# Optimization experiments

Measured on AMD Instinct MI355X. Metric: run time of the kernel, lower is better.

## Reference

```python
import jax, jax.numpy as jnp
import numpy as np

OUT, IN, BLK = 4096, 4096, 32
N_BLOCKS = OUT * IN // BLK
# FP4 magnitude lookup (E2M1): index = low 3 bits of the nibble
FP4_LOOKUP = jnp.array([0.0, 0.5, 1.0, 1.5, 2.0, 3.0, 4.0, 6.0], dtype=jnp.float32)


def setup_inputs() -> dict:
    key = jax.random.key(0)
    k1, k2, k3, k4 = jax.random.split(key, 4)
    x = jax.random.normal(k1, (4, 2048, IN), dtype=jnp.float32)
    # packed uint8 codes (stored as int32): two FP4 nibbles per byte
    quantized_weight = jax.random.randint(k2, (OUT * IN // 2,), 0, 256, dtype=jnp.int32)
    # positive per-block scales (abs-max of each 32-element block in the original)
    weight_scales = jax.random.uniform(k3, (N_BLOCKS,), dtype=jnp.float32, minval=0.01, maxval=1.0)
    bias = jax.random.normal(k4, (OUT,), dtype=jnp.float32) * 0.01
    return {"x": x, "quantized_weight": quantized_weight,
            "weight_scales": weight_scales, "bias": bias}


def _dequantize(quantized_weight, weight_scales):
    # unpack: high nibble first, then low nibble (matches _unpack_fp4 stack order)
    high = (quantized_weight >> 4) & 15
    low = quantized_weight & 15
    nibbles = jnp.stack([high, low], axis=-1).reshape(-1)  # [OUT*IN]
    # sign bit (bit 3): 1 -> negative, 0 -> positive
    sign = jnp.where(((nibbles >> 3) & 1) == 1, -1.0, 1.0).astype(jnp.float32)
    magnitude = FP4_LOOKUP[nibbles & 7]
    vals = magnitude * sign                                  # [OUT*IN]
    vals = vals.reshape(N_BLOCKS, BLK) * weight_scales[:, None]
    return vals.reshape(OUT, IN)


def reference(x, quantized_weight, weight_scales, bias):
    W = _dequantize(quantized_weight, weight_scales)  # [OUT, IN]
    # F.linear: x @ W.T + bias
    return jnp.einsum('bsi,oi->bso', x, W) + bias
```

## Files before the change

kernel.cpp:

```cpp
#include <hip/hip_runtime.h>
#include <hip/hip_bf16.h>
#include <stdint.h>


#define M_DIM 8192
#define N_DIM 4096
#define K_DIM 4096
#define NBLK_W (N_DIM * K_DIM / 32)

typedef __bf16 bf16x8 __attribute__((ext_vector_type(8)));
typedef float  f32x4  __attribute__((ext_vector_type(4)));


__device__ __forceinline__ uint16_t f32_to_bf16_rn(float f) {
  uint32_t u = __float_as_uint(f);
  uint32_t r = (u + 0x7FFFu + ((u >> 16) & 1u)) >> 16;
  return (uint16_t)r;
}
__device__ __forceinline__ uint32_t pack_bf16x2(float e0, float e1) {
  return (uint32_t)f32_to_bf16_rn(e0) | ((uint32_t)f32_to_bf16_rn(e1) << 16);
}
__device__ __forceinline__ float fp4_to_f32(int nib) {
  uint32_t e = (uint32_t)(nib >> 1) & 3u;
  uint32_t m = (uint32_t)nib & 1u;
  uint32_t s = (uint32_t)(nib >> 3) & 1u;
  uint32_t bits = e ? (((126u + e) << 23) | (m << 22)) : (m ? 0x3F000000u : 0u);
  bits |= s << 31;
  return __uint_as_float(bits);
}
__device__ __forceinline__ void gload_lds16(const void* g, void* lds) {
  __builtin_amdgcn_global_load_lds(
      (const __attribute__((address_space(1))) unsigned int*)g,
      (__attribute__((address_space(3))) unsigned int*)lds,
      16, 0, 0);
}

__global__ __launch_bounds__(256) void dequant_w(const int* __restrict__ q,
                                                 const float* __restrict__ scales,
                                                 uint32_t* __restrict__ W) {
  int b = blockIdx.x * 256 + threadIdx.x;
  float sc = scales[b];
  const int4* q4 = reinterpret_cast<const int4*>(q) + (size_t)b * 4;
  int4* dst = reinterpret_cast<int4*>(W + (size_t)b * 16);
#pragma unroll
  for (int i = 0; i < 4; ++i) {
    int4 v = q4[i];
    int b0 = v.x & 0xFF, b1 = v.y & 0xFF, b2 = v.z & 0xFF, b3 = v.w & 0xFF;
    uint32_t p0 = pack_bf16x2(fp4_to_f32((b0 >> 4) & 15) * sc, fp4_to_f32(b0 & 15) * sc);
    uint32_t p1 = pack_bf16x2(fp4_to_f32((b1 >> 4) & 15) * sc, fp4_to_f32(b1 & 15) * sc);
    uint32_t p2 = pack_bf16x2(fp4_to_f32((b2 >> 4) & 15) * sc, fp4_to_f32(b2 & 15) * sc);
    uint32_t p3 = pack_bf16x2(fp4_to_f32((b3 >> 4) & 15) * sc, fp4_to_f32(b3 & 15) * sc);
    int4 o; o.x = (int)p0; o.y = (int)p1; o.z = (int)p2; o.w = (int)p3;
    dst[i] = o;
  }
}

__global__ __launch_bounds__(256) void cvt_x(const float* __restrict__ x,
                                             uint32_t* __restrict__ xb) {
  size_t i = ((size_t)blockIdx.x * 256 + threadIdx.x) * 8;
  float4 a = *reinterpret_cast<const float4*>(x + i);
  float4 c = *reinterpret_cast<const float4*>(x + i + 4);
  int4 o;
  o.x = (int)pack_bf16x2(a.x, a.y);
  o.y = (int)pack_bf16x2(a.z, a.w);
  o.z = (int)pack_bf16x2(c.x, c.y);
  o.w = (int)pack_bf16x2(c.z, c.w);
  *reinterpret_cast<int4*>(xb + i / 2) = o;
}


#define BUF0 0
#define BUF1 65536
#define A0OFF 0
#define A1OFF 16384
#define B0OFF 32768
#define B1OFF 49152
#define AH1 (128 * 4096)
#define NITER 32

#define BARRIER()   asm volatile("s_barrier" ::: "memory")
#define WAIT_LGKM0() do { asm volatile("s_waitcnt lgkmcnt(0)" ::: "memory"); \
                          __builtin_amdgcn_sched_barrier(0); } while (0)
#define LGKM4()     do { asm volatile("s_waitcnt lgkmcnt(4)" ::: "memory"); \
                          __builtin_amdgcn_sched_barrier(0); } while (0)
#define WAIT_VM6()  asm volatile("s_waitcnt vmcnt(6)" ::: "memory")
#define WAIT_VM4()  asm volatile("s_waitcnt vmcnt(4)" ::: "memory")
#define WAIT_VM0()  asm volatile("s_waitcnt vmcnt(0)" ::: "memory")
#define PRIO1()     __builtin_amdgcn_s_setprio(1)
#define PRIO0()     __builtin_amdgcn_s_setprio(0)

#define LDA2(SET, CB, F) do {                                      \
    const uint32_t r0_ = a_rd + (F) * 2048;                        \
    const uint32_t r1_ = a_rd + ((F) + 1) * 2048;                  \
    aA[SET][0][0] = *(const bf16x8*)(smem + (CB) + r0_);           \
    aA[SET][0][1] = *(const bf16x8*)(smem + (CB) + (r0_ ^ 64));    \
    aA[SET][1][0] = *(const bf16x8*)(smem + (CB) + r1_);           \
    aA[SET][1][1] = *(const bf16x8*)(smem + (CB) + (r1_ ^ 64));    \
  } while (0)

#define LDB(CB) do {                                               \
    _Pragma("unroll")                                              \
    for (int nf_ = 0; nf_ < 4; ++nf_) {                            \
      const uint32_t r_ = b_rd + nf_ * 2048;                       \
      bfr[nf_][0] = *(const bf16x8*)(smem + (CB) + r_);            \
      bfr[nf_][1] = *(const bf16x8*)(smem + (CB) + (r_ ^ 64));     \
    }                                                              \
  } while (0)

#define MFMAQ(Q, SET) do {                                         \
    _Pragma("unroll")                                              \
    for (int nf_ = 0; nf_ < 4; ++nf_) {                            \
      _Pragma("unroll")                                            \
      for (int kk_ = 0; kk_ < 2; ++kk_) {                          \
        acc[2*(Q)][nf_] = __builtin_amdgcn_mfma_f32_16x16x32_bf16( \
            aA[SET][0][kk_], bfr[nf_][kk_], acc[2*(Q)][nf_], 0, 0, 0);   \
        acc[2*(Q)+1][nf_] = __builtin_amdgcn_mfma_f32_16x16x32_bf16(     \
            aA[SET][1][kk_], bfr[nf_][kk_], acc[2*(Q)+1][nf_], 0, 0, 0); \
      }                                                            \
    }                                                              \
  } while (0)

__device__ __forceinline__ void stage_half_tile(const __bf16* gsrc, char* lds_dst) {
  gload_lds16(gsrc, lds_dst);
  gload_lds16(gsrc + 64 * 4096, lds_dst + 8192);
}

__global__ __launch_bounds__(512, 2) void gemm256_8ph(const __bf16* __restrict__ A,
                                                      const __bf16* __restrict__ B,
                                                      const float* __restrict__ bias,
                                                      float* __restrict__ C) {
  __shared__ __align__(16) char smem[131072];

  const int t    = threadIdx.x;
  const int wave = t >> 6;
  const int lane = t & 63;
  const int l16  = lane & 15;
  const int kg   = lane >> 4;
  const int wm   = wave >> 2;
  const int wn   = wave & 3;

  const int orig = blockIdx.x;
  const int swz  = (orig & 7) * 64 + (orig >> 3);
  const int bn   = swz & 15;
  const int bm   = swz >> 4;

  const int c8 = (t & 7) ^ ((t >> 3) & 7);
  const __bf16* gA = A + ((size_t)(bm * 256 + (t >> 3))) * 4096 + c8 * 8;
  const __bf16* gB = B + ((size_t)(bn * 256 + (t >> 3))) * 4096 + c8 * 8;
  char* stw = smem + wave * 1024;

  const uint32_t ca = ((uint32_t)(kg ^ (l16 & 7))) << 4;
  const uint32_t a_rd = (uint32_t)(wm ? A1OFF : A0OFF) + (uint32_t)l16 * 128 + ca;
  const uint32_t b_rd = (uint32_t)(wn >= 2 ? B1OFF : B0OFF) +
                        (uint32_t)(wn & 1) * 8192 + (uint32_t)l16 * 128 + ca;

  f32x4 acc[8][4];
#pragma unroll
  for (int i = 0; i < 8; ++i)
#pragma unroll
    for (int j = 0; j < 4; ++j) acc[i][j] = (f32x4){0.f, 0.f, 0.f, 0.f};

  bf16x8 aA[2][2][2];
  bf16x8 bfr[4][2];

  stage_half_tile(gA,            stw + BUF0 + A0OFF);
  stage_half_tile(gA + AH1,      stw + BUF0 + A1OFF);
  stage_half_tile(gB,            stw + BUF0 + B0OFF);
  stage_half_tile(gB + AH1,      stw + BUF0 + B1OFF);
  stage_half_tile(gB + 64,       stw + BUF1 + B0OFF);
  stage_half_tile(gB + AH1 + 64, stw + BUF1 + B1OFF);
  stage_half_tile(gA + 64,       stw + BUF1 + A0OFF);
  WAIT_VM6();
  BARRIER();
  LDA2(0, BUF0, 0);

  for (int j = 0; j < NITER - 1; ++j) {
    const size_t kO  = (size_t)(2 * j + 1) * 64;
    const size_t kE2 = (size_t)(2 * j + 2) * 64;
    const size_t kO2 = (size_t)(2 * j + 3) * 64;
    WAIT_LGKM0();
    LDB(BUF0);
    LDA2(1, BUF0, 2);
    LGKM4();
    PRIO1(); MFMAQ(0, 0); PRIO0();
    stage_half_tile(gA + AH1 + kO, stw + BUF1 + A1OFF);
    BARRIER();
    WAIT_LGKM0();
    LDA2(0, BUF0, 4);
    PRIO1(); MFMAQ(1, 1); PRIO0();
    stage_half_tile(gB + kE2, stw + BUF0 + B0OFF);
    BARRIER();
    WAIT_LGKM0();
    LDA2(1, BUF0, 6);
    PRIO1(); MFMAQ(2, 0); PRIO0();
    stage_half_tile(gB + AH1 + kE2, stw + BUF0 + B1OFF);
    WAIT_VM4();
    BARRIER();
    WAIT_LGKM0();
    LDA2(0, BUF1, 0);
    PRIO1(); MFMAQ(3, 1); PRIO0();
    stage_half_tile(gA + kE2, stw + BUF0 + A0OFF);
    BARRIER();
    WAIT_LGKM0();
    LDB(BUF1);
    LDA2(1, BUF1, 2);
    LGKM4();
    PRIO1(); MFMAQ(0, 0); PRIO0();
    stage_half_tile(gA + AH1 + kE2, stw + BUF0 + A1OFF);
    BARRIER();
    WAIT_LGKM0();
    LDA2(0, BUF1, 4);
    PRIO1(); MFMAQ(1, 1); PRIO0();
    stage_half_tile(gB + kO2, stw + BUF1 + B0OFF);
    BARRIER();
    WAIT_LGKM0();
    LDA2(1, BUF1, 6);
    PRIO1(); MFMAQ(2, 0); PRIO0();
    stage_half_tile(gB + AH1 + kO2, stw + BUF1 + B1OFF);
    stage_half_tile(gA + kO2,       stw + BUF1 + A0OFF);
    WAIT_VM6();
    BARRIER();
    WAIT_LGKM0();
    LDA2(0, BUF0, 0);
    PRIO1(); MFMAQ(3, 1); PRIO0();
    BARRIER();
  }
  {
    const size_t kO = (size_t)(2 * (NITER - 1) + 1) * 64;
    WAIT_LGKM0(); LDB(BUF0); LDA2(1, BUF0, 2); LGKM4();
    PRIO1(); MFMAQ(0, 0); PRIO0();
    stage_half_tile(gA + AH1 + kO, stw + BUF1 + A1OFF);
    BARRIER();
    WAIT_LGKM0(); LDA2(0, BUF0, 4);
    PRIO1(); MFMAQ(1, 1); PRIO0();
    BARRIER();
    WAIT_LGKM0(); LDA2(1, BUF0, 6);
    PRIO1(); MFMAQ(2, 0); PRIO0();
    WAIT_VM0();
    BARRIER();
    WAIT_LGKM0(); LDA2(0, BUF1, 0);
    PRIO1(); MFMAQ(3, 1); PRIO0();
    BARRIER();
    WAIT_LGKM0(); LDB(BUF1); LDA2(1, BUF1, 2); LGKM4();
    PRIO1(); MFMAQ(0, 0); PRIO0();
    BARRIER();
    WAIT_LGKM0(); LDA2(0, BUF1, 4);
    PRIO1(); MFMAQ(1, 1); PRIO0();
    BARRIER();
    WAIT_LGKM0(); LDA2(1, BUF1, 6);
    PRIO1(); MFMAQ(2, 0); PRIO0();
    BARRIER();
    WAIT_LGKM0();
    PRIO1(); MFMAQ(3, 1); PRIO0();
  }

#pragma unroll
  for (int mf = 0; mf < 8; ++mf) {
    const int m0 = bm * 256 + wm * 128 + mf * 16 + kg * 4;
#pragma unroll
    for (int nf = 0; nf < 4; ++nf) {
      const int n = bn * 256 + wn * 64 + nf * 16 + l16;
      const float bv = bias[n];
#pragma unroll
      for (int r = 0; r < 4; ++r)
        C[(size_t)(m0 + r) * N_DIM + n] = acc[mf][nf][r] + bv;
    }
  }
}

__global__ __launch_bounds__(256) void naive_fused(const float* __restrict__ x,
                                                   const int* __restrict__ q,
                                                   const float* __restrict__ scales,
                                                   const float* __restrict__ bias,
                                                   float* __restrict__ out) {
  __shared__ float xs[K_DIM];
  const int m = blockIdx.y;
  const int n = blockIdx.x * 256 + threadIdx.x;
  for (int k = threadIdx.x; k < K_DIM; k += 256)
    xs[k] = x[(size_t)m * K_DIM + k];
  __syncthreads();

  const int4* q4 = reinterpret_cast<const int4*>(q) + (size_t)n * 512;
  float acc = 0.f, sc = 0.f;
  for (int c = 0; c < 512; ++c) {
    if ((c & 3) == 0) sc = scales[n * 128 + (c >> 2)];
    int4 v = q4[c];
    int b0 = v.x & 0xFF, b1 = v.y & 0xFF, b2 = v.z & 0xFF, b3 = v.w & 0xFF;
    int k = c * 8;
    acc += xs[k + 0] * fp4_to_f32((b0 >> 4) & 15) * sc;
    acc += xs[k + 1] * fp4_to_f32(b0 & 15) * sc;
    acc += xs[k + 2] * fp4_to_f32((b1 >> 4) & 15) * sc;
    acc += xs[k + 3] * fp4_to_f32(b1 & 15) * sc;
    acc += xs[k + 4] * fp4_to_f32((b2 >> 4) & 15) * sc;
    acc += xs[k + 5] * fp4_to_f32(b2 & 15) * sc;
    acc += xs[k + 6] * fp4_to_f32((b3 >> 4) & 15) * sc;
    acc += xs[k + 7] * fp4_to_f32(b3 & 15) * sc;
  }
  out[(size_t)m * N_DIM + n] = acc + bias[n];
}

extern "C" void kernel_launch(void* const* d_in, const int* in_sizes, int n_in,
                              void* d_out, int out_size, void* d_ws, size_t ws_size,
                              hipStream_t stream) {
  const float* x    = (const float*)d_in[0];
  const int*   q    = (const int*)d_in[1];
  const float* sc   = (const float*)d_in[2];
  const float* bias = (const float*)d_in[3];
  float* out = (float*)d_out;

  const size_t xb_bytes = (size_t)M_DIM * K_DIM * 2;
  const size_t w_bytes  = (size_t)N_DIM * K_DIM * 2;

  if (ws_size >= xb_bytes + w_bytes) {
    uint32_t* xb = (uint32_t*)d_ws;
    uint32_t* W  = (uint32_t*)((char*)d_ws + xb_bytes);

    dequant_w<<<NBLK_W / 256, 256, 0, stream>>>(q, sc, W);
    cvt_x<<<(M_DIM * (size_t)K_DIM / 8) / 256, 256, 0, stream>>>(x, xb);

    gemm256_8ph<<<dim3(512), 512, 0, stream>>>((const __bf16*)xb, (const __bf16*)W, bias, out);
  } else {
    dim3 grid(N_DIM / 256, M_DIM);
    naive_fused<<<grid, 256, 0, stream>>>(x, q, sc, bias, out);
  }
}
```

Measured before the change: 282.0 us.

## Replace eight-phase interleaved GEMM schedule with simple per-k-tile double buffering

Rewrites the GEMM main loop so that each k-tile iteration issues all global-to-LDS stages for the next tile up front, then does LDS reads and MFMAs on the current buffer. It ends with a full vmcnt(0) wait and a single barrier. This replaces the hand-interleaved eight-phase schedule with many barriers and partial waits. The aim is fewer barriers and simpler control, at the cost of a coarser overlap between global loads and compute that may expose memory latency at each tile boundary.

```diff
diff --git a/kernel.cpp b/kernel.cpp
--- a/kernel.cpp
+++ b/kernel.cpp
@@ -76,15 +76,10 @@
 #define B0OFF 32768
 #define B1OFF 49152
 #define AH1 (128 * 4096)
-#define NITER 32
 
 #define BARRIER()   asm volatile("s_barrier" ::: "memory")
-#define WAIT_LGKM0() do { asm volatile("s_waitcnt lgkmcnt(0)" ::: "memory"); \
+#define LGKMN(n)    do { asm volatile("s_waitcnt lgkmcnt(" #n ")" ::: "memory"); \
                           __builtin_amdgcn_sched_barrier(0); } while (0)
-#define LGKM4()     do { asm volatile("s_waitcnt lgkmcnt(4)" ::: "memory"); \
-                          __builtin_amdgcn_sched_barrier(0); } while (0)
-#define WAIT_VM6()  asm volatile("s_waitcnt vmcnt(6)" ::: "memory")
-#define WAIT_VM4()  asm volatile("s_waitcnt vmcnt(4)" ::: "memory")
 #define WAIT_VM0()  asm volatile("s_waitcnt vmcnt(0)" ::: "memory")
 #define PRIO1()     __builtin_amdgcn_s_setprio(1)
 #define PRIO0()     __builtin_amdgcn_s_setprio(0)
@@ -98,9 +93,9 @@
     aA[SET][1][1] = *(const bf16x8*)(smem + (CB) + (r1_ ^ 64));    \
   } while (0)
 
-#define LDB(CB) do {                                               \
+#define LDB2(CB, NF) do {                                          \
     _Pragma("unroll")                                              \
-    for (int nf_ = 0; nf_ < 4; ++nf_) {                            \
+    for (int nf_ = (NF); nf_ < (NF) + 2; ++nf_) {                  \
       const uint32_t r_ = b_rd + nf_ * 2048;                       \
       bfr[nf_][0] = *(const bf16x8*)(smem + (CB) + r_);            \
       bfr[nf_][1] = *(const bf16x8*)(smem + (CB) + (r_ ^ 64));     \
@@ -125,10 +120,34 @@
   gload_lds16(gsrc + 64 * 4096, lds_dst + 8192);
 }
 
-__global__ __launch_bounds__(512, 2) void gemm256_8ph(const __bf16* __restrict__ A,
-                                                      const __bf16* __restrict__ B,
-                                                      const float* __restrict__ bias,
-                                                      float* __restrict__ C) {
+#define ITER(CB, CBN, KN, DO_STAGE)                                \
+  do {                                                             \
+    if (DO_STAGE) {                                                \
+      stage_half_tile(gA + (KN),       stw + (CBN) + A0OFF);       \
+      stage_half_tile(gA + AH1 + (KN), stw + (CBN) + A1OFF);       \
+      stage_half_tile(gB + (KN),       stw + (CBN) + B0OFF);       \
+      stage_half_tile(gB + AH1 + (KN), stw + (CBN) + B1OFF);       \
+    }                                                              \
+    LDB2(CB, 0); LDB2(CB, 2);                                      \
+    LDA2(0, CB, 0); LDA2(1, CB, 2);                                \
+    LGKMN(4);                                                      \
+    PRIO1(); MFMAQ(0, 0); PRIO0();                                 \
+    LDA2(0, CB, 4);                                                \
+    LGKMN(4);                                                      \
+    PRIO1(); MFMAQ(1, 1); PRIO0();                                 \
+    LDA2(1, CB, 6);                                                \
+    LGKMN(4);                                                      \
+    PRIO1(); MFMAQ(2, 0); PRIO0();                                 \
+    LGKMN(0);                                                      \
+    PRIO1(); MFMAQ(3, 1); PRIO0();                                 \
+    WAIT_VM0();                                                    \
+    BARRIER();                                                     \
+  } while (0)
+
+__global__ __launch_bounds__(512, 2) void gemm256_kt(const __bf16* __restrict__ A,
+                                                     const __bf16* __restrict__ B,
+                                                     const float* __restrict__ bias,
+                                                     float* __restrict__ C) {
   __shared__ __align__(16) char smem[131072];
 
   const int t    = threadIdx.x;
@@ -163,95 +182,17 @@
   bf16x8 aA[2][2][2];
   bf16x8 bfr[4][2];
 
-  stage_half_tile(gA,            stw + BUF0 + A0OFF);
-  stage_half_tile(gA + AH1,      stw + BUF0 + A1OFF);
-  stage_half_tile(gB,            stw + BUF0 + B0OFF);
-  stage_half_tile(gB + AH1,      stw + BUF0 + B1OFF);
-  stage_half_tile(gB + 64,       stw + BUF1 + B0OFF);
-  stage_half_tile(gB + AH1 + 64, stw + BUF1 + B1OFF);
-  stage_half_tile(gA + 64,       stw + BUF1 + A0OFF);
-  WAIT_VM6();
+  stage_half_tile(gA,       stw + BUF0 + A0OFF);
+  stage_half_tile(gA + AH1, stw + BUF0 + A1OFF);
+  stage_half_tile(gB,       stw + BUF0 + B0OFF);
+  stage_half_tile(gB + AH1, stw + BUF0 + B1OFF);
+  WAIT_VM0();
   BARRIER();
-  LDA2(0, BUF0, 0);
-
-  for (int j = 0; j < NITER - 1; ++j) {
-    const size_t kO  = (size_t)(2 * j + 1) * 64;
-    const size_t kE2 = (size_t)(2 * j + 2) * 64;
-    const size_t kO2 = (size_t)(2 * j + 3) * 64;
-    WAIT_LGKM0();
-    LDB(BUF0);
-    LDA2(1, BUF0, 2);
-    LGKM4();
-    PRIO1(); MFMAQ(0, 0); PRIO0();
-    stage_half_tile(gA + AH1 + kO, stw + BUF1 + A1OFF);
-    BARRIER();
-    WAIT_LGKM0();
-    LDA2(0, BUF0, 4);
-    PRIO1(); MFMAQ(1, 1); PRIO0();
-    stage_half_tile(gB + kE2, stw + BUF0 + B0OFF);
-    BARRIER();
-    WAIT_LGKM0();
-    LDA2(1, BUF0, 6);
-    PRIO1(); MFMAQ(2, 0); PRIO0();
-    stage_half_tile(gB + AH1 + kE2, stw + BUF0 + B1OFF);
-    WAIT_VM4();
-    BARRIER();
-    WAIT_LGKM0();
-    LDA2(0, BUF1, 0);
-    PRIO1(); MFMAQ(3, 1); PRIO0();
-    stage_half_tile(gA + kE2, stw + BUF0 + A0OFF);
-    BARRIER();
-    WAIT_LGKM0();
-    LDB(BUF1);
-    LDA2(1, BUF1, 2);
-    LGKM4();
-    PRIO1(); MFMAQ(0, 0); PRIO0();
-    stage_half_tile(gA + AH1 + kE2, stw + BUF0 + A1OFF);
-    BARRIER();
-    WAIT_LGKM0();
-    LDA2(0, BUF1, 4);
-    PRIO1(); MFMAQ(1, 1); PRIO0();
-    stage_half_tile(gB + kO2, stw + BUF1 + B0OFF);
-    BARRIER();
-    WAIT_LGKM0();
-    LDA2(1, BUF1, 6);
-    PRIO1(); MFMAQ(2, 0); PRIO0();
-    stage_half_tile(gB + AH1 + kO2, stw + BUF1 + B1OFF);
-    stage_half_tile(gA + kO2,       stw + BUF1 + A0OFF);
-    WAIT_VM6();
-    BARRIER();
-    WAIT_LGKM0();
-    LDA2(0, BUF0, 0);
-    PRIO1(); MFMAQ(3, 1); PRIO0();
-    BARRIER();
-  }
-  {
-    const size_t kO = (size_t)(2 * (NITER - 1) + 1) * 64;
-    WAIT_LGKM0(); LDB(BUF0); LDA2(1, BUF0, 2); LGKM4();
-    PRIO1(); MFMAQ(0, 0); PRIO0();
-    stage_half_tile(gA + AH1 + kO, stw + BUF1 + A1OFF);
-    BARRIER();
-    WAIT_LGKM0(); LDA2(0, BUF0, 4);
-    PRIO1(); MFMAQ(1, 1); PRIO0();
-    BARRIER();
-    WAIT_LGKM0(); LDA2(1, BUF0, 6);
-    PRIO1(); MFMAQ(2, 0); PRIO0();
-    WAIT_VM0();
-    BARRIER();
-    WAIT_LGKM0(); LDA2(0, BUF1, 0);
-    PRIO1(); MFMAQ(3, 1); PRIO0();
-    BARRIER();
-    WAIT_LGKM0(); LDB(BUF1); LDA2(1, BUF1, 2); LGKM4();
-    PRIO1(); MFMAQ(0, 0); PRIO0();
-    BARRIER();
-    WAIT_LGKM0(); LDA2(0, BUF1, 4);
-    PRIO1(); MFMAQ(1, 1); PRIO0();
-    BARRIER();
-    WAIT_LGKM0(); LDA2(1, BUF1, 6);
-    PRIO1(); MFMAQ(2, 0); PRIO0();
-    BARRIER();
-    WAIT_LGKM0();
-    PRIO1(); MFMAQ(3, 1); PRIO0();
+
+  for (int j = 0; j < 32; ++j) {
+    const size_t k0 = (size_t)(2 * j) * 64;
+    ITER(BUF0, BUF1, k0 + 64, true);
+    ITER(BUF1, BUF0, k0 + 128, j < 31);
   }
 
 #pragma unroll
@@ -318,7 +259,7 @@
     dequant_w<<<NBLK_W / 256, 256, 0, stream>>>(q, sc, W);
     cvt_x<<<(M_DIM * (size_t)K_DIM / 8) / 256, 256, 0, stream>>>(x, xb);
 
-    gemm256_8ph<<<dim3(512), 512, 0, stream>>>((const __bf16*)xb, (const __bf16*)W, bias, out);
+    gemm256_kt<<<dim3(512), 512, 0, stream>>>((const __bf16*)xb, (const __bf16*)W, bias, out);
   } else {
     dim3 grid(N_DIM / 256, M_DIM);
     naive_fused<<<grid, 256, 0, stream>>>(x, q, sc, bias, out);
```

Result: no change. 285.4 us (+1.2%).

## Merge prep kernels and make GEMM blocks compute two M-tiles persistently

Applied to the files above, without the earlier changes.

Combines the weight dequantization and activation bf16 conversion into one launch, removing a kernel launch and its tail. The GEMM grid is halved to 256 blocks, and each block computes two 256-row M tiles that share the same B columns. The prologue loads for the second tile are issued during the first tile's epilogue so the pipeline stays full across tiles. In exchange, the epilogue stores of the first tile now sit on the critical path inside the block, and half as many blocks may leave CUs underused, since 256 blocks at 2 per CU is below the device's CU count.

```diff
diff --git a/kernel.cpp b/kernel.cpp
--- a/kernel.cpp
+++ b/kernel.cpp
@@ -35,37 +35,39 @@
       16, 0, 0);
 }
 
-__global__ __launch_bounds__(256) void dequant_w(const int* __restrict__ q,
-                                                 const float* __restrict__ scales,
-                                                 uint32_t* __restrict__ W) {
-  int b = blockIdx.x * 256 + threadIdx.x;
-  float sc = scales[b];
-  const int4* q4 = reinterpret_cast<const int4*>(q) + (size_t)b * 4;
-  int4* dst = reinterpret_cast<int4*>(W + (size_t)b * 16);
-#pragma unroll
-  for (int i = 0; i < 4; ++i) {
-    int4 v = q4[i];
-    int b0 = v.x & 0xFF, b1 = v.y & 0xFF, b2 = v.z & 0xFF, b3 = v.w & 0xFF;
-    uint32_t p0 = pack_bf16x2(fp4_to_f32((b0 >> 4) & 15) * sc, fp4_to_f32(b0 & 15) * sc);
-    uint32_t p1 = pack_bf16x2(fp4_to_f32((b1 >> 4) & 15) * sc, fp4_to_f32(b1 & 15) * sc);
-    uint32_t p2 = pack_bf16x2(fp4_to_f32((b2 >> 4) & 15) * sc, fp4_to_f32(b2 & 15) * sc);
-    uint32_t p3 = pack_bf16x2(fp4_to_f32((b3 >> 4) & 15) * sc, fp4_to_f32(b3 & 15) * sc);
-    int4 o; o.x = (int)p0; o.y = (int)p1; o.z = (int)p2; o.w = (int)p3;
-    dst[i] = o;
-  }
-}
-
-__global__ __launch_bounds__(256) void cvt_x(const float* __restrict__ x,
-                                             uint32_t* __restrict__ xb) {
-  size_t i = ((size_t)blockIdx.x * 256 + threadIdx.x) * 8;
-  float4 a = *reinterpret_cast<const float4*>(x + i);
-  float4 c = *reinterpret_cast<const float4*>(x + i + 4);
-  int4 o;
-  o.x = (int)pack_bf16x2(a.x, a.y);
-  o.y = (int)pack_bf16x2(a.z, a.w);
-  o.z = (int)pack_bf16x2(c.x, c.y);
-  o.w = (int)pack_bf16x2(c.z, c.w);
-  *reinterpret_cast<int4*>(xb + i / 2) = o;
+__global__ __launch_bounds__(256) void pre_all(const int* __restrict__ q,
+                                               const float* __restrict__ scales,
+                                               uint32_t* __restrict__ W,
+                                               const float* __restrict__ x,
+                                               uint32_t* __restrict__ xb) {
+  const int bid = blockIdx.x;
+  if (bid < 2048) {
+    int b = bid * 256 + threadIdx.x;
+    float sc = scales[b];
+    const int4* q4 = reinterpret_cast<const int4*>(q) + (size_t)b * 4;
+    int4* dst = reinterpret_cast<int4*>(W + (size_t)b * 16);
+#pragma unroll
+    for (int i = 0; i < 4; ++i) {
+      int4 v = q4[i];
+      int b0 = v.x & 0xFF, b1 = v.y & 0xFF, b2 = v.z & 0xFF, b3 = v.w & 0xFF;
+      uint32_t p0 = pack_bf16x2(fp4_to_f32((b0 >> 4) & 15) * sc, fp4_to_f32(b0 & 15) * sc);
+      uint32_t p1 = pack_bf16x2(fp4_to_f32((b1 >> 4) & 15) * sc, fp4_to_f32(b1 & 15) * sc);
+      uint32_t p2 = pack_bf16x2(fp4_to_f32((b2 >> 4) & 15) * sc, fp4_to_f32(b2 & 15) * sc);
+      uint32_t p3 = pack_bf16x2(fp4_to_f32((b3 >> 4) & 15) * sc, fp4_to_f32(b3 & 15) * sc);
+      int4 o; o.x = (int)p0; o.y = (int)p1; o.z = (int)p2; o.w = (int)p3;
+      dst[i] = o;
+    }
+  } else {
+    size_t i = ((size_t)(bid - 2048) * 256 + threadIdx.x) * 8;
+    float4 a = *reinterpret_cast<const float4*>(x + i);
+    float4 c = *reinterpret_cast<const float4*>(x + i + 4);
+    int4 o;
+    o.x = (int)pack_bf16x2(a.x, a.y);
+    o.y = (int)pack_bf16x2(a.z, a.w);
+    o.z = (int)pack_bf16x2(c.x, c.y);
+    o.w = (int)pack_bf16x2(c.z, c.w);
+    *reinterpret_cast<int4*>(xb + i / 2) = o;
+  }
 }
 
 
@@ -76,7 +78,6 @@
 #define B0OFF 32768
 #define B1OFF 49152
 #define AH1 (128 * 4096)
-#define NITER 32
 
 #define BARRIER()   asm volatile("s_barrier" ::: "memory")
 #define WAIT_LGKM0() do { asm volatile("s_waitcnt lgkmcnt(0)" ::: "memory"); \
@@ -125,10 +126,56 @@
   gload_lds16(gsrc + 64 * 4096, lds_dst + 8192);
 }
 
-__global__ __launch_bounds__(512, 2) void gemm256_8ph(const __bf16* __restrict__ A,
-                                                      const __bf16* __restrict__ B,
-                                                      const float* __restrict__ bias,
-                                                      float* __restrict__ C) {
+#define MAIN_PAIR(GA, kO, kE2, kO2)                                     \
+  do {                                                                  \
+                                                                \
+    WAIT_LGKM0(); LDB(BUF0); LDA2(1, BUF0, 2); LGKM4();                 \
+    PRIO1(); MFMAQ(0, 0); PRIO0();                                      \
+    stage_half_tile((GA) + AH1 + (kO), stw + BUF1 + A1OFF);             \
+    BARRIER();                                                          \
+                                                                \
+    WAIT_LGKM0(); LDA2(0, BUF0, 4);                                     \
+    PRIO1(); MFMAQ(1, 1); PRIO0();                                      \
+    stage_half_tile(gB + (kE2), stw + BUF0 + B0OFF);                    \
+    BARRIER();                                                          \
+                                                                \
+    WAIT_LGKM0(); LDA2(1, BUF0, 6);                                     \
+    PRIO1(); MFMAQ(2, 0); PRIO0();                                      \
+    stage_half_tile(gB + AH1 + (kE2), stw + BUF0 + B1OFF);              \
+    WAIT_VM4();                                                         \
+    BARRIER();                                                          \
+                                                                \
+    WAIT_LGKM0(); LDA2(0, BUF1, 0);                                     \
+    PRIO1(); MFMAQ(3, 1); PRIO0();                                      \
+    stage_half_tile((GA) + (kE2), stw + BUF0 + A0OFF);                  \
+    BARRIER();                                                          \
+                                                                \
+    WAIT_LGKM0(); LDB(BUF1); LDA2(1, BUF1, 2); LGKM4();                 \
+    PRIO1(); MFMAQ(0, 0); PRIO0();                                      \
+    stage_half_tile((GA) + AH1 + (kE2), stw + BUF0 + A1OFF);            \
+    BARRIER();                                                          \
+                                                                \
+    WAIT_LGKM0(); LDA2(0, BUF1, 4);                                     \
+    PRIO1(); MFMAQ(1, 1); PRIO0();                                      \
+    stage_half_tile(gB + (kO2), stw + BUF1 + B0OFF);                    \
+    BARRIER();                                                          \
+                                                                \
+    WAIT_LGKM0(); LDA2(1, BUF1, 6);                                     \
+    PRIO1(); MFMAQ(2, 0); PRIO0();                                      \
+    stage_half_tile(gB + AH1 + (kO2), stw + BUF1 + B1OFF);              \
+    stage_half_tile((GA) + (kO2),     stw + BUF1 + A0OFF);              \
+    WAIT_VM6();                                                         \
+    BARRIER();                                                          \
+                                                                \
+    WAIT_LGKM0(); LDA2(0, BUF0, 0);                                     \
+    PRIO1(); MFMAQ(3, 1); PRIO0();                                      \
+    BARRIER();                                                          \
+  } while (0)
+
+__global__ __launch_bounds__(512, 2) void gemm256_p2(const __bf16* __restrict__ A,
+                                                     const __bf16* __restrict__ B,
+                                                     const float* __restrict__ bias,
+                                                     float* __restrict__ C) {
   __shared__ __align__(16) char smem[131072];
 
   const int t    = threadIdx.x;
@@ -140,13 +187,14 @@
   const int wn   = wave & 3;
 
   const int orig = blockIdx.x;
-  const int swz  = (orig & 7) * 64 + (orig >> 3);
+  const int swz  = (orig & 7) * 32 + (orig >> 3);
   const int bn   = swz & 15;
   const int bm   = swz >> 4;
 
   const int c8 = (t & 7) ^ ((t >> 3) & 7);
-  const __bf16* gA = A + ((size_t)(bm * 256 + (t >> 3))) * 4096 + c8 * 8;
-  const __bf16* gB = B + ((size_t)(bn * 256 + (t >> 3))) * 4096 + c8 * 8;
+  const __bf16* gA  = A + ((size_t)(bm * 256 + (t >> 3))) * 4096 + c8 * 8;
+  const __bf16* gA2 = gA + (size_t)16 * 256 * 4096;
+  const __bf16* gB  = B + ((size_t)(bn * 256 + (t >> 3))) * 4096 + c8 * 8;
   char* stw = smem + wave * 1024;
 
   const uint32_t ca = ((uint32_t)(kg ^ (l16 & 7))) << 4;
@@ -174,65 +222,81 @@
   BARRIER();
   LDA2(0, BUF0, 0);
 
-  for (int j = 0; j < NITER - 1; ++j) {
+  for (int j = 0; j < 31; ++j) {
     const size_t kO  = (size_t)(2 * j + 1) * 64;
     const size_t kE2 = (size_t)(2 * j + 2) * 64;
     const size_t kO2 = (size_t)(2 * j + 3) * 64;
-    WAIT_LGKM0();
-    LDB(BUF0);
-    LDA2(1, BUF0, 2);
-    LGKM4();
-    PRIO1(); MFMAQ(0, 0); PRIO0();
-    stage_half_tile(gA + AH1 + kO, stw + BUF1 + A1OFF);
-    BARRIER();
-    WAIT_LGKM0();
-    LDA2(0, BUF0, 4);
-    PRIO1(); MFMAQ(1, 1); PRIO0();
-    stage_half_tile(gB + kE2, stw + BUF0 + B0OFF);
-    BARRIER();
-    WAIT_LGKM0();
-    LDA2(1, BUF0, 6);
-    PRIO1(); MFMAQ(2, 0); PRIO0();
-    stage_half_tile(gB + AH1 + kE2, stw + BUF0 + B1OFF);
-    WAIT_VM4();
-    BARRIER();
-    WAIT_LGKM0();
-    LDA2(0, BUF1, 0);
-    PRIO1(); MFMAQ(3, 1); PRIO0();
-    stage_half_tile(gA + kE2, stw + BUF0 + A0OFF);
-    BARRIER();
-    WAIT_LGKM0();
-    LDB(BUF1);
-    LDA2(1, BUF1, 2);
-    LGKM4();
-    PRIO1(); MFMAQ(0, 0); PRIO0();
-    stage_half_tile(gA + AH1 + kE2, stw + BUF0 + A1OFF);
-    BARRIER();
-    WAIT_LGKM0();
-    LDA2(0, BUF1, 4);
-    PRIO1(); MFMAQ(1, 1); PRIO0();
-    stage_half_tile(gB + kO2, stw + BUF1 + B0OFF);
-    BARRIER();
-    WAIT_LGKM0();
-    LDA2(1, BUF1, 6);
-    PRIO1(); MFMAQ(2, 0); PRIO0();
-    stage_half_tile(gB + AH1 + kO2, stw + BUF1 + B1OFF);
-    stage_half_tile(gA + kO2,       stw + BUF1 + A0OFF);
-    WAIT_VM6();
-    BARRIER();
-    WAIT_LGKM0();
-    LDA2(0, BUF0, 0);
-    PRIO1(); MFMAQ(3, 1); PRIO0();
-    BARRIER();
+    MAIN_PAIR(gA, kO, kE2, kO2);
   }
   {
-    const size_t kO = (size_t)(2 * (NITER - 1) + 1) * 64;
+    const size_t kO = (size_t)63 * 64;
     WAIT_LGKM0(); LDB(BUF0); LDA2(1, BUF0, 2); LGKM4();
     PRIO1(); MFMAQ(0, 0); PRIO0();
     stage_half_tile(gA + AH1 + kO, stw + BUF1 + A1OFF);
     BARRIER();
     WAIT_LGKM0(); LDA2(0, BUF0, 4);
     PRIO1(); MFMAQ(1, 1); PRIO0();
+    stage_half_tile(gB, stw + BUF0 + B0OFF);
+    BARRIER();
+    WAIT_LGKM0(); LDA2(1, BUF0, 6);
+    PRIO1(); MFMAQ(2, 0); PRIO0();
+    stage_half_tile(gB + AH1, stw + BUF0 + B1OFF);
+    WAIT_VM4();
+    BARRIER();
+    WAIT_LGKM0(); LDA2(0, BUF1, 0);
+    PRIO1(); MFMAQ(3, 1); PRIO0();
+    stage_half_tile(gA2, stw + BUF0 + A0OFF);
+    BARRIER();
+    WAIT_LGKM0(); LDB(BUF1); LDA2(1, BUF1, 2); LGKM4();
+    PRIO1(); MFMAQ(0, 0); PRIO0();
+    stage_half_tile(gA2 + AH1, stw + BUF0 + A1OFF);
+    BARRIER();
+    WAIT_LGKM0(); LDA2(0, BUF1, 4);
+    PRIO1(); MFMAQ(1, 1); PRIO0();
+    stage_half_tile(gB + 64, stw + BUF1 + B0OFF);
+    BARRIER();
+    WAIT_LGKM0(); LDA2(1, BUF1, 6);
+    PRIO1(); MFMAQ(2, 0); PRIO0();
+    stage_half_tile(gB + AH1 + 64, stw + BUF1 + B1OFF);
+    BARRIER();
+    WAIT_LGKM0();
+    PRIO1(); MFMAQ(3, 1); PRIO0();
+    stage_half_tile(gA2 + 64, stw + BUF1 + A0OFF);
+    WAIT_VM0();
+    BARRIER();
+  }
+#pragma unroll
+  for (int mf = 0; mf < 8; ++mf) {
+    const int m0 = bm * 256 + wm * 128 + mf * 16 + kg * 4;
+#pragma unroll
+    for (int nf = 0; nf < 4; ++nf) {
+      const int n = bn * 256 + wn * 64 + nf * 16 + l16;
+      const float bv = bias[n];
+#pragma unroll
+      for (int r = 0; r < 4; ++r)
+        C[(size_t)(m0 + r) * N_DIM + n] = acc[mf][nf][r] + bv;
+    }
+  }
+#pragma unroll
+  for (int i = 0; i < 8; ++i)
+#pragma unroll
+    for (int j = 0; j < 4; ++j) acc[i][j] = (f32x4){0.f, 0.f, 0.f, 0.f};
+  LDA2(0, BUF0, 0);
+
+  for (int j = 0; j < 31; ++j) {
+    const size_t kO  = (size_t)(2 * j + 1) * 64;
+    const size_t kE2 = (size_t)(2 * j + 2) * 64;
+    const size_t kO2 = (size_t)(2 * j + 3) * 64;
+    MAIN_PAIR(gA2, kO, kE2, kO2);
+  }
+  {
+    const size_t kO = (size_t)63 * 64;
+    WAIT_LGKM0(); LDB(BUF0); LDA2(1, BUF0, 2); LGKM4();
+    PRIO1(); MFMAQ(0, 0); PRIO0();
+    stage_half_tile(gA2 + AH1 + kO, stw + BUF1 + A1OFF);
+    BARRIER();
+    WAIT_LGKM0(); LDA2(0, BUF0, 4);
+    PRIO1(); MFMAQ(1, 1); PRIO0();
     BARRIER();
     WAIT_LGKM0(); LDA2(1, BUF0, 6);
     PRIO1(); MFMAQ(2, 0); PRIO0();
@@ -253,10 +317,9 @@
     WAIT_LGKM0();
     PRIO1(); MFMAQ(3, 1); PRIO0();
   }
-
 #pragma unroll
   for (int mf = 0; mf < 8; ++mf) {
-    const int m0 = bm * 256 + wm * 128 + mf * 16 + kg * 4;
+    const int m0 = (bm + 16) * 256 + wm * 128 + mf * 16 + kg * 4;
 #pragma unroll
     for (int nf = 0; nf < 4; ++nf) {
       const int n = bn * 256 + wn * 64 + nf * 16 + l16;
@@ -315,10 +378,8 @@
     uint32_t* xb = (uint32_t*)d_ws;
     uint32_t* W  = (uint32_t*)((char*)d_ws + xb_bytes);
 
-    dequant_w<<<NBLK_W / 256, 256, 0, stream>>>(q, sc, W);
-    cvt_x<<<(M_DIM * (size_t)K_DIM / 8) / 256, 256, 0, stream>>>(x, xb);
-
-    gemm256_8ph<<<dim3(512), 512, 0, stream>>>((const __bf16*)xb, (const __bf16*)W, bias, out);
+    pre_all<<<2048 + 16384, 256, 0, stream>>>(q, sc, W, x, xb);
+    gemm256_p2<<<dim3(256), 512, 0, stream>>>((const __bf16*)xb, (const __bf16*)W, bias, out);
   } else {
     dim3 grid(N_DIM / 256, M_DIM);
     naive_fused<<<grid, 256, 0, stream>>>(x, q, sc, bias, out);
```

Measured after the change: 276.4 us. 1.02x faster.
